# Kernel tuning notes

Measured on AMD Instinct MI355X. Metric: run time of the kernel, lower is better.

Reference implementation:

```python
import jax, jax.numpy as jnp
import numpy as np

N = 50000      # nodes
E = 800000     # edges
F_IN = 128     # input feature dim (OGBN-MAG paper features)
H = 4          # attention heads
HID = 64       # hidden_dim (per-head out channels)
HC = H * HID   # 256, concat output width
NC = 349       # num_classes
BN_EPS = 1e-5


def setup_inputs() -> dict:
    key = jax.random.key(0)
    ks = jax.random.split(key, 32)
    s = 0.05
    inp = {
        "x": jax.random.normal(ks[0], (N, F_IN), dtype=jnp.float32),
        "edge_index": jax.random.randint(ks[1], (2, E), 0, N, dtype=jnp.int64),
    }
    dins = [F_IN, HC]
    i = 2
    for l in range(2):
        d = dins[l]
        inp[f"ws{l}"] = jax.random.normal(ks[i], (d, HC), jnp.float32) * s; i += 1
        inp[f"wd{l}"] = jax.random.normal(ks[i], (d, HC), jnp.float32) * s; i += 1
        inp[f"atts{l}"] = jax.random.normal(ks[i], (H, HID), jnp.float32) * s; i += 1
        inp[f"attd{l}"] = jax.random.normal(ks[i], (H, HID), jnp.float32) * s; i += 1
        inp[f"bg{l}"] = jnp.zeros((HC,), jnp.float32); i += 1
        inp[f"lw{l}"] = jax.random.normal(ks[i], (d, HC), jnp.float32) * s; i += 1
        inp[f"lb{l}"] = jnp.zeros((HC,), jnp.float32); i += 1
        inp[f"g{l}"] = jnp.ones((HC,), jnp.float32); i += 1
        inp[f"b{l}"] = jnp.zeros((HC,), jnp.float32); i += 1
    inp["fcw"] = jax.random.normal(ks[i], (HC, NC), jnp.float32) * s
    inp["fcb"] = jnp.zeros((NC,), jnp.float32)
    return inp


def _gat(x, src, dst, ws, wd, atts, attd, bias):
    # PyG GATConv: separate src/dst projections, per-edge additive attention,
    # softmax over incoming edges of each dst node, scatter-add aggregation.
    n = x.shape[0]
    xs = (x @ ws).reshape(n, H, HID)            # [N,H,C] source messages
    xd = (x @ wd).reshape(n, H, HID)
    a_s = jnp.einsum("nhc,hc->nh", xs, atts)    # alpha_src
    a_d = jnp.einsum("nhc,hc->nh", xd, attd)    # alpha_dst
    e = jax.nn.leaky_relu(a_s[src] + a_d[dst], 0.2)   # [E,H]
    m = jax.ops.segment_max(e, dst, num_segments=n)   # segment-softmax (stable)
    ex = jnp.exp(e - m[dst])
    den = jax.ops.segment_sum(ex, dst, num_segments=n)
    w = ex / (den[dst] + 1e-16)                 # [E,H]
    out = jax.ops.segment_sum(xs[src] * w[:, :, None], dst, num_segments=n)
    return out.reshape(n, HC) + bias


def _bn(h, gamma, beta):
    # training-mode BatchNorm1d: batch statistics over nodes, biased variance
    mu = jnp.mean(h, axis=0)
    var = jnp.mean(jnp.square(h - mu), axis=0)
    return (h - mu) * jax.lax.rsqrt(var + BN_EPS) * gamma + beta


def reference(x, edge_index, ws0, wd0, atts0, attd0, bg0, lw0, lb0, g0, b0,
              ws1, wd1, atts1, attd1, bg1, lw1, lb1, g1, b1, fcw, fcb):
    src, dst = edge_index[0], edge_index[1]
    h = _gat(x, src, dst, ws0, wd0, atts0, attd0, bg0) + x @ lw0 + lb0
    h = jax.nn.relu(_bn(h, g0, b0))
    h = _gat(h, src, dst, ws1, wd1, atts1, attd1, bg1) + h @ lw1 + lb1
    h = jax.nn.relu(_bn(h, g1, b1))
    return h @ fcw + fcb
```

## Files before the change

kernel.cpp:

```cpp
#include <hip/hip_runtime.h>
#include <hip/hip_bf16.h>
#include <math.h>

#define N_NODES 50000
#define N_EDGES 800000
#define HCH 256
#define NHEAD 4
#define HIDC 64
#define NCLS 349
#define F_IN 128

typedef short short8 __attribute__((ext_vector_type(8)));
typedef float floatx4 __attribute__((ext_vector_type(4)));

__global__ void k_detect(const unsigned* ei, int* flag) {
    if (blockIdx.x == 0 && threadIdx.x == 0) {
        int i64 = 1;
        for (int e = 0; e < 64; e++)
            if (ei[2 * e + 1] != 0u) { i64 = 0; break; }
        *flag = i64;
    }
}

__device__ __forceinline__ void edge_sd(const int* ei, int e, int i64, int& s, int& d) {
    if (i64) {
        const long long* p = (const long long*)ei;
        s = (int)p[e]; d = (int)p[N_EDGES + e];
    } else {
        s = ei[e]; d = ei[N_EDGES + e];
    }
}

__global__ void k_deg(const int* ei, const int* flag, int* deg) {
    int e = blockIdx.x * 256 + threadIdx.x;
    if (e >= N_EDGES) return;
    int s, d; edge_sd(ei, e, *flag, s, d);
    atomicAdd(&deg[d], 1);
}

__global__ __launch_bounds__(256) void k_scan1(const int* __restrict__ deg,
                                               int* __restrict__ rowptr,
                                               int* __restrict__ bsum) {
    __shared__ int sd[256];
    int t = threadIdx.x;
    int base = blockIdx.x * 1024 + t * 4;
    int d0 = 0, d1 = 0, d2 = 0, d3 = 0;
    if (base + 3 < N_NODES) {
        int4 v = *(const int4*)(deg + base);
        d0 = v.x; d1 = v.y; d2 = v.z; d3 = v.w;
    } else {
        if (base + 0 < N_NODES) d0 = deg[base + 0];
        if (base + 1 < N_NODES) d1 = deg[base + 1];
        if (base + 2 < N_NODES) d2 = deg[base + 2];
        if (base + 3 < N_NODES) d3 = deg[base + 3];
    }
    int ts = d0 + d1 + d2 + d3;
    sd[t] = ts;
    __syncthreads();
    #pragma unroll
    for (int off = 1; off < 256; off <<= 1) {
        int v = (t >= off) ? sd[t - off] : 0;
        __syncthreads();
        sd[t] += v;
        __syncthreads();
    }
    int excl = (t == 0) ? 0 : sd[t - 1];
    if (base + 0 < N_NODES) rowptr[base + 0] = excl;
    if (base + 1 < N_NODES) rowptr[base + 1] = excl + d0;
    if (base + 2 < N_NODES) rowptr[base + 2] = excl + d0 + d1;
    if (base + 3 < N_NODES) rowptr[base + 3] = excl + d0 + d1 + d2;
    if (t == 255) bsum[blockIdx.x] = sd[255];
}

__global__ void k_scan2(int* __restrict__ bsum, int nb, int* __restrict__ rowptr) {
    int lane = threadIdx.x;
    int orig = (lane < nb) ? bsum[lane] : 0;
    int v = orig;
    #pragma unroll
    for (int off = 1; off < 64; off <<= 1) {
        int tv = __shfl_up(v, off, 64);
        if (lane >= off) v += tv;
    }
    if (lane < nb) bsum[lane] = v - orig;
    if (lane == 0) rowptr[N_NODES] = N_EDGES;
}

__global__ __launch_bounds__(256) void k_scan3(int* __restrict__ rowptr,
                                               const int* __restrict__ bsum) {
    int base = blockIdx.x * 1024 + threadIdx.x * 4;
    int off = bsum[blockIdx.x];
    if (base + 3 < N_NODES) {
        int4 v = *(int4*)(rowptr + base);
        v.x += off; v.y += off; v.z += off; v.w += off;
        *(int4*)(rowptr + base) = v;
    } else {
        for (int j = 0; j < 4; j++)
            if (base + j < N_NODES) rowptr[base + j] += off;
    }
}

__global__ void k_fill(const int* ei, const int* flag, const int* __restrict__ rowptr,
                       int* cursor, int* __restrict__ esrc) {
    int e = blockIdx.x * 256 + threadIdx.x;
    if (e >= N_EDGES) return;
    int s, d; edge_sd(ei, e, *flag, s, d);
    int pos = atomicAdd(&cursor[d], 1);
    esrc[rowptr[d] + pos] = s;
}

__global__ void k_wtilde(const float* __restrict__ ws, const float* __restrict__ wd,
                         const float* __restrict__ atts, const float* __restrict__ attd,
                         float* __restrict__ wt, int d) {
    int id = blockIdx.x * 256 + threadIdx.x;
    if (id >= d * 8) return;
    int j = id & 7, k = id >> 3;
    const float* w = (j < 4) ? ws : wd;
    const float* at = (j < 4) ? atts : attd;
    int h = j & 3;
    float s = 0.f;
    for (int c = 0; c < HIDC; c++) s += w[k * HCH + h * HIDC + c] * at[h * HIDC + c];
    wt[k * 8 + j] = s;
}

__device__ __forceinline__ unsigned short b16(float v) {
    __hip_bfloat16 t = __float2bfloat16(v);
    return *(unsigned short*)&t;
}

__device__ __forceinline__ float bfu(unsigned short u) {
    unsigned v = (unsigned)u << 16;
    return __builtin_bit_cast(float, v);
}

__device__ __forceinline__ void bsplit(float v, unsigned short& h, unsigned short& l) {
    __hip_bfloat16 bh = __float2bfloat16(v);
    float hv = __bfloat162float(bh);
    __hip_bfloat16 bl = __float2bfloat16(v - hv);
    h = *(unsigned short*)&bh;
    l = *(unsigned short*)&bl;
}

__global__ void k_wcat_t(const float* __restrict__ ws, const float* __restrict__ lw,
                         const float* __restrict__ wtil, int K,
                         unsigned short* __restrict__ Bh, unsigned short* __restrict__ Bl) {
    int id = blockIdx.x * 256 + threadIdx.x;
    if (id >= 640 * K) return;
    int c = id / K, k = id % K;
    float v;
    if (c < 256) v = ws[(size_t)k * 256 + c];
    else if (c < 512) v = lw[(size_t)k * 256 + (c - 256)];
    else if (c < 520) v = wtil[(size_t)k * 8 + (c - 512)];
    else v = 0.f;
    unsigned short h, l;
    bsplit(v, h, l);
    Bh[(size_t)c * K + k] = h;
    Bl[(size_t)c * K + k] = l;
}

__global__ void k_fcw_t(const float* __restrict__ fcw, int K,
                        unsigned short* __restrict__ Bh, unsigned short* __restrict__ Bl) {
    int id = blockIdx.x * 256 + threadIdx.x;
    if (id >= 384 * K) return;
    int c = id / K, k = id % K;
    float v = (c < NCLS) ? fcw[(size_t)k * NCLS + c] : 0.f;
    unsigned short h, l;
    bsplit(v, h, l);
    Bh[(size_t)c * K + k] = h;
    Bl[(size_t)c * K + k] = l;
}

__global__ __launch_bounds__(256) void k_gemm2(
    const float* __restrict__ Af32, const __hip_bfloat16* __restrict__ Ab,
    const unsigned short* __restrict__ Bh, const unsigned short* __restrict__ Bl,
    float* __restrict__ C, int ldc, __hip_bfloat16* __restrict__ xsb,
    __hip_bfloat16* __restrict__ linbb, float* __restrict__ aout,
    const float* __restrict__ bias, int M, int K, int Nc) {
    __shared__ unsigned short sA[128 * 40];
    __shared__ unsigned short sBh[128 * 40];
    __shared__ unsigned short sBl[128 * 40];
    int tid = threadIdx.x;
    int lane = tid & 63, wave = tid >> 6;
    int wm = wave >> 1, wn = wave & 1;
    int row0 = blockIdx.x * 128, col0 = blockIdx.y * 128;
    floatx4 acc[4][4] = {};
    int sr = tid >> 1;
    int sc = (tid & 1) * 2;
    int kc = lane >> 4;
    int fr = lane & 15;
    for (int k0 = 0; k0 < K; k0 += 32) {
        int4 z = {0, 0, 0, 0};
        int4 va0 = z, va1 = z;
        int gr = row0 + sr;
        if (gr < M) {
            if (Af32) {
                const float* px = Af32 + (size_t)gr * K + k0 + sc * 8;
                float4 f0 = *(const float4*)(px);
                float4 f1 = *(const float4*)(px + 4);
                float4 f2 = *(const float4*)(px + 8);
                float4 f3 = *(const float4*)(px + 12);
                float xv[16] = {f0.x, f0.y, f0.z, f0.w, f1.x, f1.y, f1.z, f1.w,
                                f2.x, f2.y, f2.z, f2.w, f3.x, f3.y, f3.z, f3.w};
                union { unsigned short us[8]; int4 v; } u0, u1;
                #pragma unroll
                for (int q = 0; q < 8; q++) {
                    u0.us[q] = b16(xv[q]);
                    u1.us[q] = b16(xv[q + 8]);
                }
                va0 = u0.v; va1 = u1.v;
            } else {
                const __hip_bfloat16* pa = Ab + (size_t)gr * K + k0 + sc * 8;
                va0 = *(const int4*)(pa);
                va1 = *(const int4*)(pa + 8);
            }
        }
        *(int4*)((char*)sA + sr * 80 + sc * 16) = va0;
        *(int4*)((char*)sA + sr * 80 + sc * 16 + 16) = va1;
        const unsigned short* pb = Bh + (size_t)(col0 + sr) * K + k0 + sc * 8;
        const unsigned short* pbl = Bl + (size_t)(col0 + sr) * K + k0 + sc * 8;
        *(int4*)((char*)sBh + sr * 80 + sc * 16) = *(const int4*)(pb);
        *(int4*)((char*)sBh + sr * 80 + sc * 16 + 16) = *(const int4*)(pb + 8);
        *(int4*)((char*)sBl + sr * 80 + sc * 16) = *(const int4*)(pbl);
        *(int4*)((char*)sBl + sr * 80 + sc * 16 + 16) = *(const int4*)(pbl + 8);
        __syncthreads();
        short8 fah[4], fbh[4], fbl[4];
        #pragma unroll
        for (int i = 0; i < 4; i++) {
            int ar = wm * 64 + i * 16 + fr;
            fah[i] = *(const short8*)((const char*)sA + ar * 80 + kc * 16);
            int bc = wn * 64 + i * 16 + fr;
            fbh[i] = *(const short8*)((const char*)sBh + bc * 80 + kc * 16);
            fbl[i] = *(const short8*)((const char*)sBl + bc * 80 + kc * 16);
        }
        #pragma unroll
        for (int i = 0; i < 4; i++)
            #pragma unroll
            for (int j = 0; j < 4; j++) {
                acc[i][j] = __builtin_amdgcn_mfma_f32_16x16x32_bf16(fah[i], fbh[j], acc[i][j], 0, 0, 0);
                acc[i][j] = __builtin_amdgcn_mfma_f32_16x16x32_bf16(fah[i], fbl[j], acc[i][j], 0, 0, 0);
            }
        __syncthreads();
    }
    #pragma unroll
    for (int i = 0; i < 4; i++) {
        #pragma unroll
        for (int j = 0; j < 4; j++) {
            int c = col0 + wn * 64 + j * 16 + fr;
            if (c >= Nc) continue;
            float bv = bias ? bias[c] : 0.f;
            #pragma unroll
            for (int q = 0; q < 4; q++) {
                int r = row0 + wm * 64 + i * 16 + (lane >> 4) * 4 + q;
                if (r >= M) continue;
                float val = acc[i][j][q] + bv;
                if (C) C[(size_t)r * ldc + c] = val;
                else if (c < 256) xsb[(size_t)r * 256 + c] = __float2bfloat16(val);
                else if (c < 512) linbb[(size_t)r * 256 + (c - 256)] = __float2bfloat16(val);
                else aout[(size_t)r * 8 + (c - 512)] = val;
            }
        }
    }
}

#define LEAKY_EXP(vv) __expf(((vv) > 0.f) ? (vv) : 0.2f * (vv))

__global__ __launch_bounds__(256) void k_agg(
    const __hip_bfloat16* __restrict__ xsb,
    const __hip_bfloat16* __restrict__ linb, const float* __restrict__ a,
    const int* __restrict__ rowptr, const int* __restrict__ esrc,
    const float* __restrict__ bg, const float* __restrict__ lb,
    __hip_bfloat16* __restrict__ hout) {
    int wave = threadIdx.x >> 6;
    int lane = threadIdx.x & 63;
    int n = blockIdx.x * 4 + wave;
    if (n >= N_NODES) return;
    int h = lane >> 4;
    int c0 = lane * 4;
    float ad = a[(size_t)n * 8 + 4 + h];
    int beg = rowptr[n], end = rowptr[n + 1];
    float a0 = 0.f, a1 = 0.f, a2 = 0.f, a3 = 0.f, dsum = 0.f;
    int k = beg;
    for (; k + 8 <= end; k += 8) {
        int s[8];
        #pragma unroll
        for (int u = 0; u < 8; u++) s[u] = esrc[k + u];
        ushort4 m[8];
        #pragma unroll
        for (int u = 0; u < 8; u++)
            m[u] = *(const ushort4*)(xsb + (size_t)s[u] * 256 + c0);
        float av[8];
        #pragma unroll
        for (int u = 0; u < 8; u++) av[u] = a[(size_t)s[u] * 8 + h];
        #pragma unroll
        for (int u = 0; u < 8; u++) {
            float ev = LEAKY_EXP(av[u] + ad);
            a0 += bfu(m[u].x) * ev;
            a1 += bfu(m[u].y) * ev;
            a2 += bfu(m[u].z) * ev;
            a3 += bfu(m[u].w) * ev;
            dsum += ev;
        }
    }
    for (; k < end; k++) {
        int s = esrc[k];
        ushort4 m = *(const ushort4*)(xsb + (size_t)s * 256 + c0);
        float ev = LEAKY_EXP(a[(size_t)s * 8 + h] + ad);
        a0 += bfu(m.x) * ev;
        a1 += bfu(m.y) * ev;
        a2 += bfu(m.z) * ev;
        a3 += bfu(m.w) * ev;
        dsum += ev;
    }
    float inv = 1.f / (dsum + 1e-16f);
    float4 bgv = *(const float4*)(bg + c0);
    float4 lbv = *(const float4*)(lb + c0);
    ushort4 lnv = *(const ushort4*)(linb + (size_t)n * 256 + c0);
    ushort4 o;
    o.x = b16(a0 * inv + bgv.x + bfu(lnv.x) + lbv.x);
    o.y = b16(a1 * inv + bgv.y + bfu(lnv.y) + lbv.y);
    o.z = b16(a2 * inv + bgv.z + bfu(lnv.z) + lbv.z);
    o.w = b16(a3 * inv + bgv.w + bfu(lnv.w) + lbv.w);
    *(ushort4*)(hout + (size_t)n * 256 + c0) = o;
}

__global__ void k_bnstats(const __hip_bfloat16* __restrict__ hb,
                          float* __restrict__ bnsum, float* __restrict__ bnsq) {
    int c = threadIdx.x;
    float s = 0.f, q = 0.f;
    for (int r = blockIdx.x; r < N_NODES; r += gridDim.x) {
        float v = __bfloat162float(hb[(size_t)r * 256 + c]);
        s += v; q += v * v;
    }
    atomicAdd(&bnsum[c], s);
    atomicAdd(&bnsq[c], q);
}

__global__ __launch_bounds__(256) void k_bnapply(
    const __hip_bfloat16* __restrict__ hb, __hip_bfloat16* __restrict__ hpost,
    const float* __restrict__ bnsum, const float* __restrict__ bnsq,
    const float* __restrict__ g, const float* __restrict__ b) {
    __shared__ float sA[256], sB[256];
    int t = threadIdx.x;
    {
        float m = bnsum[t] / (float)N_NODES;
        float v = bnsq[t] / (float)N_NODES - m * m;
        float rs = rsqrtf(v + 1e-5f) * g[t];
        sA[t] = rs;
        sB[t] = b[t] - m * rs;
    }
    __syncthreads();
    size_t tot = (size_t)N_NODES * 256;
    for (size_t i = (size_t)blockIdx.x * 256 + t; i < tot;
         i += (size_t)gridDim.x * 256) {
        int c = (int)(i & 255);
        float v = __bfloat162float(hb[i]) * sA[c] + sB[c];
        v = v > 0.f ? v : 0.f;
        hpost[i] = __float2bfloat16(v);
    }
}

extern "C" void kernel_launch(void* const* d_in, const int* in_sizes, int n_in,
                              void* d_out, int out_size, void* d_ws, size_t ws_size,
                              hipStream_t stream) {
    const float* x     = (const float*)d_in[0];
    const int*   ei    = (const int*)d_in[1];
    const float* ws0   = (const float*)d_in[2];
    const float* wd0   = (const float*)d_in[3];
    const float* atts0 = (const float*)d_in[4];
    const float* attd0 = (const float*)d_in[5];
    const float* bg0   = (const float*)d_in[6];
    const float* lw0   = (const float*)d_in[7];
    const float* lb0   = (const float*)d_in[8];
    const float* g0    = (const float*)d_in[9];
    const float* b0    = (const float*)d_in[10];
    const float* ws1   = (const float*)d_in[11];
    const float* wd1   = (const float*)d_in[12];
    const float* atts1 = (const float*)d_in[13];
    const float* attd1 = (const float*)d_in[14];
    const float* bg1   = (const float*)d_in[15];
    const float* lw1   = (const float*)d_in[16];
    const float* lb1   = (const float*)d_in[17];
    const float* g1    = (const float*)d_in[18];
    const float* b1    = (const float*)d_in[19];
    const float* fcw   = (const float*)d_in[20];
    const float* fcb   = (const float*)d_in[21];
    float* out = (float*)d_out;

    char* p = (char*)d_ws;
    auto alloc = [&](size_t bytes) -> char* {
        char* r = p;
        p += (bytes + 255) & ~(size_t)255;
        return r;
    };
    __hip_bfloat16* xsb   = (__hip_bfloat16*)alloc((size_t)N_NODES * 256 * 2);
    __hip_bfloat16* linb  = (__hip_bfloat16*)alloc((size_t)N_NODES * 256 * 2);
    __hip_bfloat16* hb    = (__hip_bfloat16*)alloc((size_t)N_NODES * 256 * 2);
    __hip_bfloat16* hpost = (__hip_bfloat16*)alloc((size_t)N_NODES * 256 * 2);
    float* a      = (float*)alloc((size_t)N_NODES * 8 * 4);
    int*   esrc   = (int*)alloc((size_t)N_EDGES * 4);
    int*   rowptr = (int*)alloc((size_t)(N_NODES + 1) * 4);
    int*   bsum   = (int*)alloc(64 * 4);
    unsigned short* w0h = (unsigned short*)alloc((size_t)640 * 128 * 2);
    unsigned short* w0l = (unsigned short*)alloc((size_t)640 * 128 * 2);
    unsigned short* w1h = (unsigned short*)alloc((size_t)640 * 256 * 2);
    unsigned short* w1l = (unsigned short*)alloc((size_t)640 * 256 * 2);
    unsigned short* fch = (unsigned short*)alloc((size_t)384 * 256 * 2);
    unsigned short* fcl = (unsigned short*)alloc((size_t)384 * 256 * 2);
    float* wtil   = (float*)alloc((size_t)256 * 8 * 4);
    int*   flag   = (int*)alloc(256);
    size_t zr_bytes = (size_t)N_NODES * 4 * 2 + 4 * 256 * 4;
    char* zbase = alloc(zr_bytes);
    int*   deg    = (int*)zbase;
    int*   cursor = deg + N_NODES;
    float* bnsum0 = (float*)(cursor + N_NODES);
    float* bnsq0  = bnsum0 + 256;
    float* bnsum1 = bnsq0 + 256;
    float* bnsq1  = bnsum1 + 256;

    hipMemsetAsync(zbase, 0, zr_bytes, stream);

    const int EB = (N_EDGES + 255) / 256;
    const int RB = (N_NODES + 127) / 128;
    const int AB = (N_NODES + 3) / 4;
    const int SB = (N_NODES + 1023) / 1024;

    k_detect<<<1, 1, 0, stream>>>((const unsigned*)ei, flag);
    k_deg<<<EB, 256, 0, stream>>>(ei, flag, deg);
    k_scan1<<<SB, 256, 0, stream>>>(deg, rowptr, bsum);
    k_scan2<<<1, 64, 0, stream>>>(bsum, SB, rowptr);
    k_scan3<<<SB, 256, 0, stream>>>(rowptr, bsum);
    k_fill<<<EB, 256, 0, stream>>>(ei, flag, rowptr, cursor, esrc);

    k_wtilde<<<(128 * 8 + 255) / 256, 256, 0, stream>>>(ws0, wd0, atts0, attd0, wtil, 128);
    k_wcat_t<<<(640 * 128 + 255) / 256, 256, 0, stream>>>(ws0, lw0, wtil, 128, w0h, w0l);
    k_wtilde<<<(256 * 8 + 255) / 256, 256, 0, stream>>>(ws1, wd1, atts1, attd1, wtil, 256);
    k_wcat_t<<<(640 * 256 + 255) / 256, 256, 0, stream>>>(ws1, lw1, wtil, 256, w1h, w1l);
    k_fcw_t<<<(384 * 256 + 255) / 256, 256, 0, stream>>>(fcw, 256, fch, fcl);

    k_gemm2<<<dim3(RB, 5), 256, 0, stream>>>(x, nullptr, w0h, w0l,
                                             nullptr, 0, xsb, linb, a,
                                             nullptr, N_NODES, 128, 520);
    k_agg<<<AB, 256, 0, stream>>>(xsb, linb, a, rowptr, esrc, bg0, lb0, hb);
    k_bnstats<<<256, 256, 0, stream>>>(hb, bnsum0, bnsq0);
    k_bnapply<<<2048, 256, 0, stream>>>(hb, hpost, bnsum0, bnsq0, g0, b0);

    k_gemm2<<<dim3(RB, 5), 256, 0, stream>>>(nullptr, hpost, w1h, w1l,
                                             nullptr, 0, xsb, linb, a,
                                             nullptr, N_NODES, 256, 520);
    k_agg<<<AB, 256, 0, stream>>>(xsb, linb, a, rowptr, esrc, bg1, lb1, hb);
    k_bnstats<<<256, 256, 0, stream>>>(hb, bnsum1, bnsq1);
    k_bnapply<<<2048, 256, 0, stream>>>(hb, hpost, bnsum1, bnsq1, g1, b1);

    k_gemm2<<<dim3(RB, 3), 256, 0, stream>>>(nullptr, hpost, fch, fcl,
                                             out, NCLS, nullptr, nullptr, nullptr,
                                             fcb, N_NODES, 256, NCLS);
}
```

Baseline: 559.8 us.

## Load GEMM tiles with direct global-to-LDS copies and XOR-swizzled layout

The GEMM's tile loading now uses global_load_lds 16-byte direct copies into shared memory, with an XOR swizzle replacing the padded 80-byte row stride to avoid bank conflicts. The fp32 input x is pre-cast to bf16 in a separate kernel, so the GEMM has only one A-operand path. The A buffers are padded to a multiple of 128 rows to drop the bounds checks. This removes register staging and in-loop conversion, but adds an extra pass over x and reads padded rows that are never written.

After: 545.8 us. 2.5% less time.

```diff
diff --git a/kernel.cpp b/kernel.cpp
--- a/kernel.cpp
+++ b/kernel.cpp
@@ -3,6 +3,7 @@
 #include <math.h>
 
 #define N_NODES 50000
+#define MPAD 50048
 #define N_EDGES 800000
 #define HCH 256
 #define NHEAD 4
@@ -140,6 +141,17 @@
     l = *(unsigned short*)&bl;
 }
 
+__global__ __launch_bounds__(256) void k_xcast(const float* __restrict__ x,
+                                               unsigned short* __restrict__ xb) {
+    size_t tot = (size_t)N_NODES * 128 / 4;
+    for (size_t i = (size_t)blockIdx.x * 256 + threadIdx.x; i < tot;
+         i += (size_t)gridDim.x * 256) {
+        float4 v = *(const float4*)(x + i * 4);
+        ushort4 o = {b16(v.x), b16(v.y), b16(v.z), b16(v.w)};
+        *(ushort4*)(xb + i * 4) = o;
+    }
+}
+
 __global__ void k_wcat_t(const float* __restrict__ ws, const float* __restrict__ lw,
                          const float* __restrict__ wtil, int K,
                          unsigned short* __restrict__ Bh, unsigned short* __restrict__ Bl) {
@@ -169,67 +181,65 @@
     Bl[(size_t)c * K + k] = l;
 }
 
+__device__ __forceinline__ void gload16(const void* g, void* l) {
+    __builtin_amdgcn_global_load_lds(
+        (const __attribute__((address_space(1))) void*)g,
+        (__attribute__((address_space(3))) void*)l, 16, 0, 0);
+}
+
 __global__ __launch_bounds__(256) void k_gemm2(
-    const float* __restrict__ Af32, const __hip_bfloat16* __restrict__ Ab,
+    const unsigned short* __restrict__ Ab,
     const unsigned short* __restrict__ Bh, const unsigned short* __restrict__ Bl,
     float* __restrict__ C, int ldc, __hip_bfloat16* __restrict__ xsb,
     __hip_bfloat16* __restrict__ linbb, float* __restrict__ aout,
     const float* __restrict__ bias, int M, int K, int Nc) {
-    __shared__ unsigned short sA[128 * 40];
-    __shared__ unsigned short sBh[128 * 40];
-    __shared__ unsigned short sBl[128 * 40];
+    __shared__ unsigned short sA[4096];
+    __shared__ unsigned short sBh[4096];
+    __shared__ unsigned short sBl[4096];
     int tid = threadIdx.x;
     int lane = tid & 63, wave = tid >> 6;
     int wm = wave >> 1, wn = wave & 1;
     int row0 = blockIdx.x * 128, col0 = blockIdx.y * 128;
+
+    int rowq[2], kcq[2];
+    #pragma unroll
+    for (int q = 0; q < 2; q++) {
+        int lds16 = wave * 128 + q * 64 + lane;
+        int line = lds16 >> 3;
+        int slot0 = (lds16 & 7) ^ (line & 7);
+        rowq[q] = (line << 1) | (slot0 >> 2);
+        kcq[q] = slot0 & 3;
+    }
+    int kc = lane >> 4, fr = lane & 15;
+    int offA[4], offB[4];
+    #pragma unroll
+    for (int i = 0; i < 4; i++) {
+        int ar = wm * 64 + i * 16 + fr;
+        int ln = ar >> 1;
+        int sl = (((ar & 1) << 2) | kc) ^ (ln & 7);
+        offA[i] = ln * 128 + sl * 16;
+        int bc = wn * 64 + i * 16 + fr;
+        ln = bc >> 1;
+        sl = (((bc & 1) << 2) | kc) ^ (ln & 7);
+        offB[i] = ln * 128 + sl * 16;
+    }
+
     floatx4 acc[4][4] = {};
-    int sr = tid >> 1;
-    int sc = (tid & 1) * 2;
-    int kc = lane >> 4;
-    int fr = lane & 15;
     for (int k0 = 0; k0 < K; k0 += 32) {
-        int4 z = {0, 0, 0, 0};
-        int4 va0 = z, va1 = z;
-        int gr = row0 + sr;
-        if (gr < M) {
-            if (Af32) {
-                const float* px = Af32 + (size_t)gr * K + k0 + sc * 8;
-                float4 f0 = *(const float4*)(px);
-                float4 f1 = *(const float4*)(px + 4);
-                float4 f2 = *(const float4*)(px + 8);
-                float4 f3 = *(const float4*)(px + 12);
-                float xv[16] = {f0.x, f0.y, f0.z, f0.w, f1.x, f1.y, f1.z, f1.w,
-                                f2.x, f2.y, f2.z, f2.w, f3.x, f3.y, f3.z, f3.w};
-                union { unsigned short us[8]; int4 v; } u0, u1;
-                #pragma unroll
-                for (int q = 0; q < 8; q++) {
-                    u0.us[q] = b16(xv[q]);
-                    u1.us[q] = b16(xv[q + 8]);
-                }
-                va0 = u0.v; va1 = u1.v;
-            } else {
-                const __hip_bfloat16* pa = Ab + (size_t)gr * K + k0 + sc * 8;
-                va0 = *(const int4*)(pa);
-                va1 = *(const int4*)(pa + 8);
-            }
+        #pragma unroll
+        for (int q = 0; q < 2; q++) {
+            int lb = wave * 2048 + q * 1024;
+            gload16(Ab + (size_t)(row0 + rowq[q]) * K + k0 + kcq[q] * 8, (char*)sA + lb);
+            gload16(Bh + (size_t)(col0 + rowq[q]) * K + k0 + kcq[q] * 8, (char*)sBh + lb);
+            gload16(Bl + (size_t)(col0 + rowq[q]) * K + k0 + kcq[q] * 8, (char*)sBl + lb);
         }
-        *(int4*)((char*)sA + sr * 80 + sc * 16) = va0;
-        *(int4*)((char*)sA + sr * 80 + sc * 16 + 16) = va1;
-        const unsigned short* pb = Bh + (size_t)(col0 + sr) * K + k0 + sc * 8;
-        const unsigned short* pbl = Bl + (size_t)(col0 + sr) * K + k0 + sc * 8;
-        *(int4*)((char*)sBh + sr * 80 + sc * 16) = *(const int4*)(pb);
-        *(int4*)((char*)sBh + sr * 80 + sc * 16 + 16) = *(const int4*)(pb + 8);
-        *(int4*)((char*)sBl + sr * 80 + sc * 16) = *(const int4*)(pbl);
-        *(int4*)((char*)sBl + sr * 80 + sc * 16 + 16) = *(const int4*)(pbl + 8);
         __syncthreads();
         short8 fah[4], fbh[4], fbl[4];
         #pragma unroll
         for (int i = 0; i < 4; i++) {
-            int ar = wm * 64 + i * 16 + fr;
-            fah[i] = *(const short8*)((const char*)sA + ar * 80 + kc * 16);
-            int bc = wn * 64 + i * 16 + fr;
-            fbh[i] = *(const short8*)((const char*)sBh + bc * 80 + kc * 16);
-            fbl[i] = *(const short8*)((const char*)sBl + bc * 80 + kc * 16);
+            fah[i] = *(const short8*)((const char*)sA + offA[i]);
+            fbh[i] = *(const short8*)((const char*)sBh + offB[i]);
+            fbl[i] = *(const short8*)((const char*)sBl + offB[i]);
         }
         #pragma unroll
         for (int i = 0; i < 4; i++)
@@ -394,7 +404,8 @@
     __hip_bfloat16* xsb   = (__hip_bfloat16*)alloc((size_t)N_NODES * 256 * 2);
     __hip_bfloat16* linb  = (__hip_bfloat16*)alloc((size_t)N_NODES * 256 * 2);
     __hip_bfloat16* hb    = (__hip_bfloat16*)alloc((size_t)N_NODES * 256 * 2);
-    __hip_bfloat16* hpost = (__hip_bfloat16*)alloc((size_t)N_NODES * 256 * 2);
+    __hip_bfloat16* hpost = (__hip_bfloat16*)alloc((size_t)MPAD * 256 * 2);
+    unsigned short* xb    = (unsigned short*)alloc((size_t)MPAD * 128 * 2);
     float* a      = (float*)alloc((size_t)N_NODES * 8 * 4);
     int*   esrc   = (int*)alloc((size_t)N_EDGES * 4);
     int*   rowptr = (int*)alloc((size_t)(N_NODES + 1) * 4);
@@ -419,7 +430,7 @@
     hipMemsetAsync(zbase, 0, zr_bytes, stream);
 
     const int EB = (N_EDGES + 255) / 256;
-    const int RB = (N_NODES + 127) / 128;
+    const int RB = MPAD / 128;
     const int AB = (N_NODES + 3) / 4;
     const int SB = (N_NODES + 1023) / 1024;
 
@@ -435,22 +446,23 @@
     k_wtilde<<<(256 * 8 + 255) / 256, 256, 0, stream>>>(ws1, wd1, atts1, attd1, wtil, 256);
     k_wcat_t<<<(640 * 256 + 255) / 256, 256, 0, stream>>>(ws1, lw1, wtil, 256, w1h, w1l);
     k_fcw_t<<<(384 * 256 + 255) / 256, 256, 0, stream>>>(fcw, 256, fch, fcl);
-
-    k_gemm2<<<dim3(RB, 5), 256, 0, stream>>>(x, nullptr, w0h, w0l,
+    k_xcast<<<2048, 256, 0, stream>>>(x, xb);
+
+    k_gemm2<<<dim3(RB, 5), 256, 0, stream>>>(xb, w0h, w0l,
                                              nullptr, 0, xsb, linb, a,
                                              nullptr, N_NODES, 128, 520);
     k_agg<<<AB, 256, 0, stream>>>(xsb, linb, a, rowptr, esrc, bg0, lb0, hb);
     k_bnstats<<<256, 256, 0, stream>>>(hb, bnsum0, bnsq0);
     k_bnapply<<<2048, 256, 0, stream>>>(hb, hpost, bnsum0, bnsq0, g0, b0);
 
-    k_gemm2<<<dim3(RB, 5), 256, 0, stream>>>(nullptr, hpost, w1h, w1l,
+    k_gemm2<<<dim3(RB, 5), 256, 0, stream>>>((const unsigned short*)hpost, w1h, w1l,
                                              nullptr, 0, xsb, linb, a,
                                              nullptr, N_NODES, 256, 520);
     k_agg<<<AB, 256, 0, stream>>>(xsb, linb, a, rowptr, esrc, bg1, lb1, hb);
     k_bnstats<<<256, 256, 0, stream>>>(hb, bnsum1, bnsq1);
     k_bnapply<<<2048, 256, 0, stream>>>(hb, hpost, bnsum1, bnsq1, g1, b1);
 
-    k_gemm2<<<dim3(RB, 3), 256, 0, stream>>>(nullptr, hpost, fch, fcl,
+    k_gemm2<<<dim3(RB, 3), 256, 0, stream>>>((const unsigned short*)hpost, fch, fcl,
                                              out, NCLS, nullptr, nullptr, nullptr,
                                              fcb, N_NODES, 256, NCLS);
 }
```
